# Kernel optimization log

Measured on AMD Instinct MI355X. Metric: run time of the kernel, lower is better.

The kernel has to match this reference:

```python
import jax, jax.numpy as jnp
import numpy as np

N_NODES = 100000
N_EDGES = 3200000
C = 256
NEG_SLOPE = 0.2


def setup_inputs() -> dict:
    key = jax.random.key(0)
    k1, k2, k3, k4 = jax.random.split(key, 4)
    x = jax.random.normal(k1, (N_NODES, C), dtype=jnp.float32)
    # xavier_uniform on (2C, 1): bound = sqrt(6/(2C+1))
    bound = float(np.sqrt(6.0 / (2 * C + 1)))
    att = jax.random.uniform(k2, (2 * C, 1), dtype=jnp.float32, minval=-bound, maxval=bound)
    row = jax.random.randint(k3, (N_EDGES,), 0, N_NODES, dtype=jnp.int64)
    col = jax.random.randint(k4, (N_EDGES,), 0, N_NODES, dtype=jnp.int64)
    edge_index = jnp.stack([row, col], axis=0)
    return {"x": x, "att": att, "edge_index": edge_index}


def reference(x, att, edge_index):
    # Original: alpha = leaky_relu(cat([x[row], x[col]], -1) @ att)
    # Equivalent split form avoids materializing the [E, 2C] concat:
    # alpha_e = (x @ att[:C])[row] + (x @ att[C:])[col]
    row, col = edge_index[0], edge_index[1]
    n = x.shape[0]
    c = x.shape[1]
    s_src = (x @ att[:c]).squeeze(-1)  # (N,)
    s_dst = (x @ att[c:]).squeeze(-1)  # (N,)
    alpha = jax.nn.leaky_relu(s_src[row] + s_dst[col], negative_slope=NEG_SLOPE)  # (E,)
    # scatter_softmax over edges grouped by destination row id
    m = jax.ops.segment_max(alpha, row, num_segments=n)          # (N,)
    e = jnp.exp(alpha - m[row])                                   # (E,)
    denom = jax.ops.segment_sum(e, row, num_segments=n)          # (N,)
    out = e / denom[row]                                          # (E,)
    # torch code transposes [E,1] -> [1,E] before scatter_softmax; squeeze(-1) is a no-op
    return out[None, :]
```

## Files before the change

kernel.cpp:

```cpp
#include <hip/hip_runtime.h>

#define NN 100000
#define NE 3200000
#define CC 256
#define NEG_SLOPE 0.2f

#define SEG_S 64
#define SEG_P 4
#define PART_SZ 25000
#define SEG_BLOCK 1024
#define ESLICE (NE / SEG_S)

typedef __attribute__((ext_vector_type(8))) _Float16 half8;

__global__ __launch_bounds__(256) void node_scores_kernel(
    const float* __restrict__ x,
    const float* __restrict__ att,
    float* __restrict__ s_src,
    float* __restrict__ s_dst) {
  int t    = blockIdx.x * blockDim.x + threadIdx.x;
  int node = t >> 4;
  int gl   = t & 15;
  if (node >= NN) return;
  const float4* xr = (const float4*)(x + (size_t)node * CC) + gl * 4;
  const float4* a0 = (const float4*)att + gl * 4;
  const float4* a1 = (const float4*)(att + CC) + gl * 4;
  float s0 = 0.f, s1 = 0.f;
#pragma unroll
  for (int j = 0; j < 4; ++j) {
    float4 xv = xr[j];
    float4 av = a0[j];
    float4 bv = a1[j];
    s0 += xv.x * av.x + xv.y * av.y + xv.z * av.z + xv.w * av.w;
    s1 += xv.x * bv.x + xv.y * bv.y + xv.z * bv.z + xv.w * bv.w;
  }
#pragma unroll
  for (int m = 8; m >= 1; m >>= 1) {
    s0 += __shfl_xor(s0, m, 64);
    s1 += __shfl_xor(s1, m, 64);
  }
  if (gl == 0) {
    s_src[node] = s0;
    s_dst[node] = s1;
  }
}

__global__ __launch_bounds__(256) void edge_exp_kernel(
    const int4* __restrict__ row4,
    const int4* __restrict__ col4,
    const float* __restrict__ s_src,
    const float* __restrict__ s_dst,
    half8* __restrict__ e_out) {
  int i = blockIdx.x * blockDim.x + threadIdx.x;
  if (i >= NE / 8) return;
  int4 ra = row4[2 * i], rb = row4[2 * i + 1];
  int4 ca = col4[2 * i], cb = col4[2 * i + 1];
  float a0 = s_src[ra.x] + s_dst[ca.x];
  float a1 = s_src[ra.y] + s_dst[ca.y];
  float a2 = s_src[ra.z] + s_dst[ca.z];
  float a3 = s_src[ra.w] + s_dst[ca.w];
  float a4 = s_src[rb.x] + s_dst[cb.x];
  float a5 = s_src[rb.y] + s_dst[cb.y];
  float a6 = s_src[rb.z] + s_dst[cb.z];
  float a7 = s_src[rb.w] + s_dst[cb.w];
  a0 = (a0 > 0.0f) ? a0 : NEG_SLOPE * a0;
  a1 = (a1 > 0.0f) ? a1 : NEG_SLOPE * a1;
  a2 = (a2 > 0.0f) ? a2 : NEG_SLOPE * a2;
  a3 = (a3 > 0.0f) ? a3 : NEG_SLOPE * a3;
  a4 = (a4 > 0.0f) ? a4 : NEG_SLOPE * a4;
  a5 = (a5 > 0.0f) ? a5 : NEG_SLOPE * a5;
  a6 = (a6 > 0.0f) ? a6 : NEG_SLOPE * a6;
  a7 = (a7 > 0.0f) ? a7 : NEG_SLOPE * a7;
  half8 h;
  h[0] = (_Float16)__expf(a0);
  h[1] = (_Float16)__expf(a1);
  h[2] = (_Float16)__expf(a2);
  h[3] = (_Float16)__expf(a3);
  h[4] = (_Float16)__expf(a4);
  h[5] = (_Float16)__expf(a5);
  h[6] = (_Float16)__expf(a6);
  h[7] = (_Float16)__expf(a7);
  e_out[i] = h;
}

__global__ __launch_bounds__(SEG_BLOCK) void segsum_kernel(
    const int* __restrict__ row,
    const _Float16* __restrict__ e,
    float* __restrict__ partial ) {
  __shared__ float lds[PART_SZ];
  int s = blockIdx.x;
  int p = blockIdx.y;
  for (int i = threadIdx.x; i < PART_SZ; i += SEG_BLOCK) lds[i] = 0.0f;
  __syncthreads();
  int lo = p * PART_SZ;
  const int4*  row4 = (const int4*)(row + s * ESLICE);
  const half8* e8   = (const half8*)(e + (size_t)s * ESLICE);
  const int n8 = ESLICE / 8;
  for (int i = threadIdx.x; i < n8; i += SEG_BLOCK) {
    int4 ra = row4[2 * i], rb = row4[2 * i + 1];
    half8 ev = e8[i];
    int r0 = ra.x - lo; if ((unsigned)r0 < PART_SZ) atomicAdd(&lds[r0], (float)ev[0]);
    int r1 = ra.y - lo; if ((unsigned)r1 < PART_SZ) atomicAdd(&lds[r1], (float)ev[1]);
    int r2 = ra.z - lo; if ((unsigned)r2 < PART_SZ) atomicAdd(&lds[r2], (float)ev[2]);
    int r3 = ra.w - lo; if ((unsigned)r3 < PART_SZ) atomicAdd(&lds[r3], (float)ev[3]);
    int r4 = rb.x - lo; if ((unsigned)r4 < PART_SZ) atomicAdd(&lds[r4], (float)ev[4]);
    int r5 = rb.y - lo; if ((unsigned)r5 < PART_SZ) atomicAdd(&lds[r5], (float)ev[5]);
    int r6 = rb.z - lo; if ((unsigned)r6 < PART_SZ) atomicAdd(&lds[r6], (float)ev[6]);
    int r7 = rb.w - lo; if ((unsigned)r7 < PART_SZ) atomicAdd(&lds[r7], (float)ev[7]);
  }
  __syncthreads();
  float* outp = partial + (size_t)s * NN + lo;
  for (int i = threadIdx.x; i < PART_SZ; i += SEG_BLOCK) outp[i] = lds[i];
}

__global__ __launch_bounds__(256) void reduce_kernel(
    const float* __restrict__ partial,
    float* __restrict__ denom) {
  int n4 = blockIdx.x * blockDim.x + threadIdx.x;
  if (n4 >= NN / 4) return;
  float4 sum = make_float4(0.f, 0.f, 0.f, 0.f);
#pragma unroll 8
  for (int s = 0; s < SEG_S; ++s) {
    float4 v = ((const float4*)(partial + (size_t)s * NN))[n4];
    sum.x += v.x; sum.y += v.y; sum.z += v.z; sum.w += v.w;
  }
  ((float4*)denom)[n4] = make_float4(1.f / sum.x, 1.f / sum.y, 1.f / sum.z, 1.f / sum.w);
}

__global__ __launch_bounds__(256) void edge_div_kernel(
    const int4* __restrict__ row4,
    const half8* __restrict__ e,
    const float* __restrict__ denom,
    float4* __restrict__ out4) {
  int i = blockIdx.x * blockDim.x + threadIdx.x;
  if (i >= NE / 8) return;
  int4 ra = row4[2 * i], rb = row4[2 * i + 1];
  half8 ev = e[i];
  float4 oa, ob;
  oa.x = (float)ev[0] * denom[ra.x];
  oa.y = (float)ev[1] * denom[ra.y];
  oa.z = (float)ev[2] * denom[ra.z];
  oa.w = (float)ev[3] * denom[ra.w];
  ob.x = (float)ev[4] * denom[rb.x];
  ob.y = (float)ev[5] * denom[rb.y];
  ob.z = (float)ev[6] * denom[rb.z];
  ob.w = (float)ev[7] * denom[rb.w];
  out4[2 * i]     = oa;
  out4[2 * i + 1] = ob;
}

extern "C" void kernel_launch(void* const* d_in, const int* in_sizes, int n_in,
                              void* d_out, int out_size, void* d_ws, size_t ws_size,
                              hipStream_t stream) {
  const float* x   = (const float*)d_in[0];
  const float* att = (const float*)d_in[1];
  const int* ei    = (const int*)d_in[2];
  const int* row   = ei;
  const int4* row4 = (const int4*)ei;
  const int4* col4 = (const int4*)(ei + NE);
  float4* out4     = (float4*)d_out;

  float* s_src    = (float*)d_ws;
  float* s_dst    = s_src + NN;
  float* denom    = s_dst + NN;
  _Float16* e_buf = (_Float16*)(denom + NN);
  float* partial  = (float*)(e_buf + NE);

  node_scores_kernel<<<(NN * 16 + 255) / 256, 256, 0, stream>>>(x, att, s_src, s_dst);
  edge_exp_kernel<<<(NE / 8 + 255) / 256, 256, 0, stream>>>(
      row4, col4, s_src, s_dst, (half8*)e_buf);
  dim3 seg_grid(SEG_S, SEG_P);
  segsum_kernel<<<seg_grid, SEG_BLOCK, 0, stream>>>(row, e_buf, partial);
  reduce_kernel<<<(NN / 4 + 255) / 256, 256, 0, stream>>>(partial, denom);
  edge_div_kernel<<<(NE / 8 + 255) / 256, 256, 0, stream>>>(
      row4, (const half8*)e_buf, denom, out4);
}
```

Measured before the change: 239.4 us.

## Fuse edge exp into partitioned segment-sum and stage gathers in LDS

Result: faster. 232.8 us (-2.8%).

```diff
diff --git a/kernel.cpp b/kernel.cpp
--- a/kernel.cpp
+++ b/kernel.cpp
@@ -5,11 +5,17 @@
 #define CC 256
 #define NEG_SLOPE 0.2f
 
-#define SEG_S 64
-#define SEG_P 4
-#define PART_SZ 25000
-#define SEG_BLOCK 1024
-#define ESLICE (NE / SEG_S)
+#define CS_S 32
+#define CS_P 8
+#define CS_PART 12500
+#define CS_ESL (NE / CS_S)
+
+#define EN_S 64
+#define EN_P 4
+#define EN_PART 25000
+#define EN_ESL (NE / EN_S)
+
+#define BLK 1024
 
 typedef __attribute__((ext_vector_type(8))) _Float16 half8;
 
@@ -45,72 +51,56 @@
   }
 }
 
-__global__ __launch_bounds__(256) void edge_exp_kernel(
-    const int4* __restrict__ row4,
-    const int4* __restrict__ col4,
+__global__ __launch_bounds__(BLK) void fused_segsum_kernel(
+    const int* __restrict__ row,
+    const int* __restrict__ col,
     const float* __restrict__ s_src,
     const float* __restrict__ s_dst,
-    half8* __restrict__ e_out) {
-  int i = blockIdx.x * blockDim.x + threadIdx.x;
-  if (i >= NE / 8) return;
-  int4 ra = row4[2 * i], rb = row4[2 * i + 1];
-  int4 ca = col4[2 * i], cb = col4[2 * i + 1];
-  float a0 = s_src[ra.x] + s_dst[ca.x];
-  float a1 = s_src[ra.y] + s_dst[ca.y];
-  float a2 = s_src[ra.z] + s_dst[ca.z];
-  float a3 = s_src[ra.w] + s_dst[ca.w];
-  float a4 = s_src[rb.x] + s_dst[cb.x];
-  float a5 = s_src[rb.y] + s_dst[cb.y];
-  float a6 = s_src[rb.z] + s_dst[cb.z];
-  float a7 = s_src[rb.w] + s_dst[cb.w];
-  a0 = (a0 > 0.0f) ? a0 : NEG_SLOPE * a0;
-  a1 = (a1 > 0.0f) ? a1 : NEG_SLOPE * a1;
-  a2 = (a2 > 0.0f) ? a2 : NEG_SLOPE * a2;
-  a3 = (a3 > 0.0f) ? a3 : NEG_SLOPE * a3;
-  a4 = (a4 > 0.0f) ? a4 : NEG_SLOPE * a4;
-  a5 = (a5 > 0.0f) ? a5 : NEG_SLOPE * a5;
-  a6 = (a6 > 0.0f) ? a6 : NEG_SLOPE * a6;
-  a7 = (a7 > 0.0f) ? a7 : NEG_SLOPE * a7;
-  half8 h;
-  h[0] = (_Float16)__expf(a0);
-  h[1] = (_Float16)__expf(a1);
-  h[2] = (_Float16)__expf(a2);
-  h[3] = (_Float16)__expf(a3);
-  h[4] = (_Float16)__expf(a4);
-  h[5] = (_Float16)__expf(a5);
-  h[6] = (_Float16)__expf(a6);
-  h[7] = (_Float16)__expf(a7);
-  e_out[i] = h;
-}
-
-__global__ __launch_bounds__(SEG_BLOCK) void segsum_kernel(
-    const int* __restrict__ row,
-    const _Float16* __restrict__ e,
+    _Float16* __restrict__ e_out,
     float* __restrict__ partial ) {
-  __shared__ float lds[PART_SZ];
-  int s = blockIdx.x;
-  int p = blockIdx.y;
-  for (int i = threadIdx.x; i < PART_SZ; i += SEG_BLOCK) lds[i] = 0.0f;
-  __syncthreads();
-  int lo = p * PART_SZ;
-  const int4*  row4 = (const int4*)(row + s * ESLICE);
-  const half8* e8   = (const half8*)(e + (size_t)s * ESLICE);
-  const int n8 = ESLICE / 8;
-  for (int i = threadIdx.x; i < n8; i += SEG_BLOCK) {
-    int4 ra = row4[2 * i], rb = row4[2 * i + 1];
-    half8 ev = e8[i];
-    int r0 = ra.x - lo; if ((unsigned)r0 < PART_SZ) atomicAdd(&lds[r0], (float)ev[0]);
-    int r1 = ra.y - lo; if ((unsigned)r1 < PART_SZ) atomicAdd(&lds[r1], (float)ev[1]);
-    int r2 = ra.z - lo; if ((unsigned)r2 < PART_SZ) atomicAdd(&lds[r2], (float)ev[2]);
-    int r3 = ra.w - lo; if ((unsigned)r3 < PART_SZ) atomicAdd(&lds[r3], (float)ev[3]);
-    int r4 = rb.x - lo; if ((unsigned)r4 < PART_SZ) atomicAdd(&lds[r4], (float)ev[4]);
-    int r5 = rb.y - lo; if ((unsigned)r5 < PART_SZ) atomicAdd(&lds[r5], (float)ev[5]);
-    int r6 = rb.z - lo; if ((unsigned)r6 < PART_SZ) atomicAdd(&lds[r6], (float)ev[6]);
-    int r7 = rb.w - lo; if ((unsigned)r7 < PART_SZ) atomicAdd(&lds[r7], (float)ev[7]);
+  __shared__ float src_lds[CS_PART];
+  __shared__ float acc[CS_PART];
+  int s  = blockIdx.x;
+  int p  = blockIdx.y;
+  int lo = p * CS_PART;
+  for (int i = threadIdx.x; i < CS_PART; i += BLK) {
+    src_lds[i] = s_src[lo + i];
+    acc[i]     = 0.0f;
   }
   __syncthreads();
+  const int4* row4 = (const int4*)(row + s * CS_ESL);
+  const int4* col4 = (const int4*)(col + s * CS_ESL);
+  _Float16* eo = e_out + (size_t)s * CS_ESL;
+  const int n8 = CS_ESL / 8;
+
+#define CS_SLOT(r, c, j)                                   \
+  do {                                                     \
+    int rr = (r)-lo;                                       \
+    if ((unsigned)rr < CS_PART) {                          \
+      float a = src_lds[rr] + s_dst[(c)];                  \
+      a = (a > 0.0f) ? a : NEG_SLOPE * a;                  \
+      _Float16 h = (_Float16)__expf(a);                    \
+      eo[8 * i + (j)] = h;                                 \
+      atomicAdd(&acc[rr], (float)h);                       \
+    }                                                      \
+  } while (0)
+
+  for (int i = threadIdx.x; i < n8; i += BLK) {
+    int4 ra = row4[2 * i], rb = row4[2 * i + 1];
+    int4 ca = col4[2 * i], cb = col4[2 * i + 1];
+    CS_SLOT(ra.x, ca.x, 0);
+    CS_SLOT(ra.y, ca.y, 1);
+    CS_SLOT(ra.z, ca.z, 2);
+    CS_SLOT(ra.w, ca.w, 3);
+    CS_SLOT(rb.x, cb.x, 4);
+    CS_SLOT(rb.y, cb.y, 5);
+    CS_SLOT(rb.z, cb.z, 6);
+    CS_SLOT(rb.w, cb.w, 7);
+  }
+#undef CS_SLOT
+  __syncthreads();
   float* outp = partial + (size_t)s * NN + lo;
-  for (int i = threadIdx.x; i < PART_SZ; i += SEG_BLOCK) outp[i] = lds[i];
+  for (int i = threadIdx.x; i < CS_PART; i += BLK) outp[i] = acc[i];
 }
 
 __global__ __launch_bounds__(256) void reduce_kernel(
@@ -120,33 +110,49 @@
   if (n4 >= NN / 4) return;
   float4 sum = make_float4(0.f, 0.f, 0.f, 0.f);
 #pragma unroll 8
-  for (int s = 0; s < SEG_S; ++s) {
+  for (int s = 0; s < CS_S; ++s) {
     float4 v = ((const float4*)(partial + (size_t)s * NN))[n4];
     sum.x += v.x; sum.y += v.y; sum.z += v.z; sum.w += v.w;
   }
   ((float4*)denom)[n4] = make_float4(1.f / sum.x, 1.f / sum.y, 1.f / sum.z, 1.f / sum.w);
 }
 
-__global__ __launch_bounds__(256) void edge_div_kernel(
-    const int4* __restrict__ row4,
-    const half8* __restrict__ e,
+__global__ __launch_bounds__(BLK) void norm_kernel(
+    const int* __restrict__ row,
+    const _Float16* __restrict__ e,
     const float* __restrict__ denom,
-    float4* __restrict__ out4) {
-  int i = blockIdx.x * blockDim.x + threadIdx.x;
-  if (i >= NE / 8) return;
-  int4 ra = row4[2 * i], rb = row4[2 * i + 1];
-  half8 ev = e[i];
-  float4 oa, ob;
-  oa.x = (float)ev[0] * denom[ra.x];
-  oa.y = (float)ev[1] * denom[ra.y];
-  oa.z = (float)ev[2] * denom[ra.z];
-  oa.w = (float)ev[3] * denom[ra.w];
-  ob.x = (float)ev[4] * denom[rb.x];
-  ob.y = (float)ev[5] * denom[rb.y];
-  ob.z = (float)ev[6] * denom[rb.z];
-  ob.w = (float)ev[7] * denom[rb.w];
-  out4[2 * i]     = oa;
-  out4[2 * i + 1] = ob;
+    float* __restrict__ out) {
+  __shared__ float d_lds[EN_PART];
+  int s  = blockIdx.x;
+  int p  = blockIdx.y;
+  int lo = p * EN_PART;
+  for (int i = threadIdx.x; i < EN_PART; i += BLK) d_lds[i] = denom[lo + i];
+  __syncthreads();
+  const int4*  row4 = (const int4*)(row + s * EN_ESL);
+  const half8* e8   = (const half8*)(e + (size_t)s * EN_ESL);
+  float* op = out + (size_t)s * EN_ESL;
+  const int n8 = EN_ESL / 8;
+
+#define EN_SLOT(r, v, j)                                   \
+  do {                                                     \
+    int rr = (r)-lo;                                       \
+    if ((unsigned)rr < EN_PART)                            \
+      op[8 * i + (j)] = (float)(v)*d_lds[rr];              \
+  } while (0)
+
+  for (int i = threadIdx.x; i < n8; i += BLK) {
+    int4 ra = row4[2 * i], rb = row4[2 * i + 1];
+    half8 ev = e8[i];
+    EN_SLOT(ra.x, ev[0], 0);
+    EN_SLOT(ra.y, ev[1], 1);
+    EN_SLOT(ra.z, ev[2], 2);
+    EN_SLOT(ra.w, ev[3], 3);
+    EN_SLOT(rb.x, ev[4], 4);
+    EN_SLOT(rb.y, ev[5], 5);
+    EN_SLOT(rb.z, ev[6], 6);
+    EN_SLOT(rb.w, ev[7], 7);
+  }
+#undef EN_SLOT
 }
 
 extern "C" void kernel_launch(void* const* d_in, const int* in_sizes, int n_in,
@@ -156,9 +162,8 @@
   const float* att = (const float*)d_in[1];
   const int* ei    = (const int*)d_in[2];
   const int* row   = ei;
-  const int4* row4 = (const int4*)ei;
-  const int4* col4 = (const int4*)(ei + NE);
-  float4* out4     = (float4*)d_out;
+  const int* col   = ei + NE;
+  float* out       = (float*)d_out;
 
   float* s_src    = (float*)d_ws;
   float* s_dst    = s_src + NN;
@@ -167,11 +172,10 @@
   float* partial  = (float*)(e_buf + NE);
 
   node_scores_kernel<<<(NN * 16 + 255) / 256, 256, 0, stream>>>(x, att, s_src, s_dst);
-  edge_exp_kernel<<<(NE / 8 + 255) / 256, 256, 0, stream>>>(
-      row4, col4, s_src, s_dst, (half8*)e_buf);
-  dim3 seg_grid(SEG_S, SEG_P);
-  segsum_kernel<<<seg_grid, SEG_BLOCK, 0, stream>>>(row, e_buf, partial);
+  dim3 cs_grid(CS_S, CS_P);
+  fused_segsum_kernel<<<cs_grid, BLK, 0, stream>>>(
+      row, col, s_src, s_dst, e_buf, partial);
   reduce_kernel<<<(NN / 4 + 255) / 256, 256, 0, stream>>>(partial, denom);
-  edge_div_kernel<<<(NE / 8 + 255) / 256, 256, 0, stream>>>(
-      row4, (const half8*)e_buf, denom, out4);
+  dim3 en_grid(EN_S, EN_P);
+  norm_kernel<<<en_grid, BLK, 0, stream>>>(row, e_buf, denom, out);
 }
```

## Fuse edge exp computation into the partitioned LDS segment-sum kernel

Applied to the files above, without the earlier changes.

After: 231.8 us. 3.2% less time.

```diff
diff --git a/kernel.cpp b/kernel.cpp
--- a/kernel.cpp
+++ b/kernel.cpp
@@ -5,11 +5,11 @@
 #define CC 256
 #define NEG_SLOPE 0.2f
 
-#define SEG_S 64
-#define SEG_P 4
-#define PART_SZ 25000
-#define SEG_BLOCK 1024
-#define ESLICE (NE / SEG_S)
+#define FS_S 80
+#define FS_P 3
+#define FS_PART 40000
+#define FS_ESL (NE / FS_S)
+#define BLK 1024
 
 typedef __attribute__((ext_vector_type(8))) _Float16 half8;
 
@@ -45,72 +45,53 @@
   }
 }
 
-__global__ __launch_bounds__(256) void edge_exp_kernel(
-    const int4* __restrict__ row4,
-    const int4* __restrict__ col4,
+__global__ __launch_bounds__(BLK) void fused_segsum_kernel(
+    const int* __restrict__ row,
+    const int* __restrict__ col,
     const float* __restrict__ s_src,
     const float* __restrict__ s_dst,
-    half8* __restrict__ e_out) {
-  int i = blockIdx.x * blockDim.x + threadIdx.x;
-  if (i >= NE / 8) return;
-  int4 ra = row4[2 * i], rb = row4[2 * i + 1];
-  int4 ca = col4[2 * i], cb = col4[2 * i + 1];
-  float a0 = s_src[ra.x] + s_dst[ca.x];
-  float a1 = s_src[ra.y] + s_dst[ca.y];
-  float a2 = s_src[ra.z] + s_dst[ca.z];
-  float a3 = s_src[ra.w] + s_dst[ca.w];
-  float a4 = s_src[rb.x] + s_dst[cb.x];
-  float a5 = s_src[rb.y] + s_dst[cb.y];
-  float a6 = s_src[rb.z] + s_dst[cb.z];
-  float a7 = s_src[rb.w] + s_dst[cb.w];
-  a0 = (a0 > 0.0f) ? a0 : NEG_SLOPE * a0;
-  a1 = (a1 > 0.0f) ? a1 : NEG_SLOPE * a1;
-  a2 = (a2 > 0.0f) ? a2 : NEG_SLOPE * a2;
-  a3 = (a3 > 0.0f) ? a3 : NEG_SLOPE * a3;
-  a4 = (a4 > 0.0f) ? a4 : NEG_SLOPE * a4;
-  a5 = (a5 > 0.0f) ? a5 : NEG_SLOPE * a5;
-  a6 = (a6 > 0.0f) ? a6 : NEG_SLOPE * a6;
-  a7 = (a7 > 0.0f) ? a7 : NEG_SLOPE * a7;
-  half8 h;
-  h[0] = (_Float16)__expf(a0);
-  h[1] = (_Float16)__expf(a1);
-  h[2] = (_Float16)__expf(a2);
-  h[3] = (_Float16)__expf(a3);
-  h[4] = (_Float16)__expf(a4);
-  h[5] = (_Float16)__expf(a5);
-  h[6] = (_Float16)__expf(a6);
-  h[7] = (_Float16)__expf(a7);
-  e_out[i] = h;
-}
+    _Float16* __restrict__ e_out,
+    float* __restrict__ partial ) {
+  __shared__ float acc[FS_PART];
+  int s  = blockIdx.x;
+  int p  = blockIdx.y;
+  int lo = p * FS_PART;
+  for (int i = threadIdx.x; i < FS_PART; i += BLK) acc[i] = 0.0f;
+  __syncthreads();
+  const int4* row4 = (const int4*)(row + s * FS_ESL);
+  const int*  cols = col + s * FS_ESL;
+  _Float16* eo = e_out + (size_t)s * FS_ESL;
+  const int n8 = FS_ESL / 8;
 
-__global__ __launch_bounds__(SEG_BLOCK) void segsum_kernel(
-    const int* __restrict__ row,
-    const _Float16* __restrict__ e,
-    float* __restrict__ partial ) {
-  __shared__ float lds[PART_SZ];
-  int s = blockIdx.x;
-  int p = blockIdx.y;
-  for (int i = threadIdx.x; i < PART_SZ; i += SEG_BLOCK) lds[i] = 0.0f;
+#define FS_SLOT(r, j)                                      \
+  do {                                                     \
+    int rr = (r)-lo;                                       \
+    if ((unsigned)rr < FS_PART) {                          \
+      float a = s_src[(r)] + s_dst[cols[8 * i + (j)]];     \
+      a = (a > 0.0f) ? a : NEG_SLOPE * a;                  \
+      _Float16 h = (_Float16)__expf(a);                    \
+      eo[8 * i + (j)] = h;                                 \
+      atomicAdd(&acc[rr], (float)h);                       \
+    }                                                      \
+  } while (0)
+
+  for (int i = threadIdx.x; i < n8; i += BLK) {
+    int4 ra = row4[2 * i], rb = row4[2 * i + 1];
+    FS_SLOT(ra.x, 0);
+    FS_SLOT(ra.y, 1);
+    FS_SLOT(ra.z, 2);
+    FS_SLOT(ra.w, 3);
+    FS_SLOT(rb.x, 4);
+    FS_SLOT(rb.y, 5);
+    FS_SLOT(rb.z, 6);
+    FS_SLOT(rb.w, 7);
+  }
+#undef FS_SLOT
   __syncthreads();
-  int lo = p * PART_SZ;
-  const int4*  row4 = (const int4*)(row + s * ESLICE);
-  const half8* e8   = (const half8*)(e + (size_t)s * ESLICE);
-  const int n8 = ESLICE / 8;
-  for (int i = threadIdx.x; i < n8; i += SEG_BLOCK) {
-    int4 ra = row4[2 * i], rb = row4[2 * i + 1];
-    half8 ev = e8[i];
-    int r0 = ra.x - lo; if ((unsigned)r0 < PART_SZ) atomicAdd(&lds[r0], (float)ev[0]);
-    int r1 = ra.y - lo; if ((unsigned)r1 < PART_SZ) atomicAdd(&lds[r1], (float)ev[1]);
-    int r2 = ra.z - lo; if ((unsigned)r2 < PART_SZ) atomicAdd(&lds[r2], (float)ev[2]);
-    int r3 = ra.w - lo; if ((unsigned)r3 < PART_SZ) atomicAdd(&lds[r3], (float)ev[3]);
-    int r4 = rb.x - lo; if ((unsigned)r4 < PART_SZ) atomicAdd(&lds[r4], (float)ev[4]);
-    int r5 = rb.y - lo; if ((unsigned)r5 < PART_SZ) atomicAdd(&lds[r5], (float)ev[5]);
-    int r6 = rb.z - lo; if ((unsigned)r6 < PART_SZ) atomicAdd(&lds[r6], (float)ev[6]);
-    int r7 = rb.w - lo; if ((unsigned)r7 < PART_SZ) atomicAdd(&lds[r7], (float)ev[7]);
-  }
-  __syncthreads();
+  int cnt = NN - lo;
+  if (cnt > FS_PART) cnt = FS_PART;
   float* outp = partial + (size_t)s * NN + lo;
-  for (int i = threadIdx.x; i < PART_SZ; i += SEG_BLOCK) outp[i] = lds[i];
+  for (int i = threadIdx.x; i < cnt; i += BLK) outp[i] = acc[i];
 }
 
 __global__ __launch_bounds__(256) void reduce_kernel(
@@ -120,7 +101,7 @@
   if (n4 >= NN / 4) return;
   float4 sum = make_float4(0.f, 0.f, 0.f, 0.f);
 #pragma unroll 8
-  for (int s = 0; s < SEG_S; ++s) {
+  for (int s = 0; s < FS_S; ++s) {
     float4 v = ((const float4*)(partial + (size_t)s * NN))[n4];
     sum.x += v.x; sum.y += v.y; sum.z += v.z; sum.w += v.w;
   }
@@ -156,8 +137,8 @@
   const float* att = (const float*)d_in[1];
   const int* ei    = (const int*)d_in[2];
   const int* row   = ei;
+  const int* col   = ei + NE;
   const int4* row4 = (const int4*)ei;
-  const int4* col4 = (const int4*)(ei + NE);
   float4* out4     = (float4*)d_out;
 
   float* s_src    = (float*)d_ws;
@@ -167,10 +148,9 @@
   float* partial  = (float*)(e_buf + NE);
 
   node_scores_kernel<<<(NN * 16 + 255) / 256, 256, 0, stream>>>(x, att, s_src, s_dst);
-  edge_exp_kernel<<<(NE / 8 + 255) / 256, 256, 0, stream>>>(
-      row4, col4, s_src, s_dst, (half8*)e_buf);
-  dim3 seg_grid(SEG_S, SEG_P);
-  segsum_kernel<<<seg_grid, SEG_BLOCK, 0, stream>>>(row, e_buf, partial);
+  dim3 fs_grid(FS_S, FS_P);
+  fused_segsum_kernel<<<fs_grid, BLK, 0, stream>>>(
+      row, col, s_src, s_dst, e_buf, partial);
   reduce_kernel<<<(NN / 4 + 255) / 256, 256, 0, stream>>>(partial, denom);
   edge_div_kernel<<<(NE / 8 + 255) / 256, 256, 0, stream>>>(
       row4, (const half8*)e_buf, denom, out4);
```
